# Kernel optimization log

Hardware: AMD Instinct MI355X
Metric: run time of the kernel (lower is better)

The kernel has to match this reference:

```python
import jax, jax.numpy as jnp
import numpy as np

EMBED_DIM = 768
MAX_LEN = 1024
ALPHA = 0.99
BATCH = 16


def setup_inputs() -> dict:
    key = jax.random.key(0)
    k1, k2, k3 = jax.random.split(key, 3)
    x = jax.random.normal(k1, (BATCH, MAX_LEN, EMBED_DIM), dtype=jnp.float32)
    # torch nn.Linear(embed_dim, 3*embed_dim): store weight as [in, out] for x @ W
    scale = 1.0 / np.sqrt(EMBED_DIM)
    W_qkv = jax.random.uniform(k2, (EMBED_DIM, 3 * EMBED_DIM), dtype=jnp.float32,
                               minval=-scale, maxval=scale)
    b_qkv = jax.random.uniform(k3, (3 * EMBED_DIM,), dtype=jnp.float32,
                               minval=-scale, maxval=scale)
    return {"x": x, "W_qkv": W_qkv, "b_qkv": b_qkv}


def _retention_mask(sl, alpha, dtype):
    # M[i, j] = alpha**(i - j) if i >= j else 0 (causal tril * decay)
    i = jnp.arange(sl)[:, None]
    j = jnp.arange(sl)[None, :]
    causal = i >= j
    # compute decay only where causal to avoid huge alpha**(negative) values
    exponent = jnp.where(causal, (i - j).astype(dtype), 0.0)
    decay = jnp.asarray(alpha, dtype) ** exponent
    return jnp.where(causal, decay, jnp.zeros((), dtype))


def reference(x, W_qkv, b_qkv):
    bs, sl, d = x.shape
    qkv = x @ W_qkv + b_qkv                      # [B, S, 3D]
    q, k, v = jnp.split(qkv, 3, axis=-1)         # each [B, S, D]
    M = _retention_mask(sl, ALPHA, x.dtype)      # [S, S]
    scores = jnp.einsum('bsd,btd->bst', q, k) / jnp.sqrt(jnp.asarray(d, x.dtype))
    out = jnp.einsum('bst,btd->bsd', scores * M[None, :, :], v)
    return out
```

## Files before the change

kernel.cpp:

```cpp
#include <hip/hip_runtime.h>
#include <hip/hip_bf16.h>


#define SEQ   1024
#define DIM   768
#define ND3   2304

typedef __attribute__((ext_vector_type(8))) short bf16x8;
typedef __attribute__((ext_vector_type(4))) float f32x4;

#define L2A     (-0.014499569695115089f)
#define RSQRTD  (0.03608439182435161f)

__device__ __forceinline__ unsigned short f2bf(float x) {
  union { float f; unsigned u; } v; v.f = x;
  unsigned r = v.u + 0x7FFFu + ((v.u >> 16) & 1u);
  return (unsigned short)(r >> 16);
}

__device__ __forceinline__ void gload16(const void* g, void* l) {
  __builtin_amdgcn_global_load_lds(
      (const __attribute__((address_space(1))) void*)g,
      (__attribute__((address_space(3))) void*)l, 16, 0, 0);
}

__device__ __forceinline__ void gemm_core(
    const unsigned short* gA, const unsigned short* gA2,
    const unsigned short* gB, const unsigned short* gB2,
    char* lsA, char* lsB, int nt, int wid, int lane, f32x4 acc[2][4]) {
  int lr = lane & 15, lg = lane >> 4;
  int wm = wid >> 1, wn = wid & 1;
  int rdA = (wm * 32 + lr) * 128 + ((lg ^ (lr & 7)) << 4);
  int rdB = (wn * 64 + lr) * 128 + ((lg ^ (lr & 7)) << 4);
  int wo = wid * 2048;

#define STAGE(t, par) do {                                                    \
    int lo_ = ((par) << 14) + wo;                                             \
    gload16(gA  + (size_t)(t) * 64, lsA + lo_);                               \
    gload16(gA2 + (size_t)(t) * 64, lsA + lo_ + 1024);                        \
    gload16(gB  + (size_t)(t) * 64, lsB + lo_);                               \
    gload16(gB2 + (size_t)(t) * 64, lsB + lo_ + 1024);                        \
  } while (0)

  STAGE(0, 0);
  STAGE(1, 1);
  asm volatile("s_waitcnt vmcnt(4)" ::: "memory");
  __builtin_amdgcn_s_barrier();
  asm volatile("" ::: "memory");

  for (int t = 0; t < nt; ++t) {
    int pbase = (t & 1) << 14;
    bf16x8 aF[2][2], bF[2][4];
#pragma unroll
    for (int kh = 0; kh < 2; ++kh) {
#pragma unroll
      for (int f = 0; f < 2; ++f)
        aF[kh][f] = *(const bf16x8*)(lsA + pbase + ((rdA + f * 2048) ^ (kh << 6)));
#pragma unroll
      for (int n = 0; n < 4; ++n)
        bF[kh][n] = *(const bf16x8*)(lsB + pbase + ((rdB + n * 2048) ^ (kh << 6)));
    }
    __builtin_amdgcn_s_setprio(1);
#pragma unroll
    for (int kh = 0; kh < 2; ++kh)
#pragma unroll
      for (int f = 0; f < 2; ++f)
#pragma unroll
        for (int n = 0; n < 4; ++n)
          acc[f][n] = __builtin_amdgcn_mfma_f32_16x16x32_bf16(aF[kh][f], bF[kh][n], acc[f][n], 0, 0, 0);
    __builtin_amdgcn_s_setprio(0);

    if (t == nt - 1) break;
    __builtin_amdgcn_s_barrier();
    asm volatile("" ::: "memory");
    if (t + 2 < nt) {
      STAGE(t + 2, t & 1);
      asm volatile("s_waitcnt vmcnt(4)" ::: "memory");
    } else {
      asm volatile("s_waitcnt vmcnt(0)" ::: "memory");
    }
    __builtin_amdgcn_s_barrier();
    asm volatile("" ::: "memory");
  }
#undef STAGE
}

__global__ void prep(const float* __restrict__ x, unsigned short* __restrict__ xb,
                     const float* __restrict__ W, unsigned short* __restrict__ Wt) {
  __shared__ float tile[64][65];
  int bid = blockIdx.x;
  if (bid < 6144) {
    size_t i = ((size_t)bid * 256 + threadIdx.x) * 8;
    float4 f0 = *(const float4*)(x + i);
    float4 f1 = *(const float4*)(x + i + 4);
    bf16x8 v;
    v[0] = (short)f2bf(f0.x); v[1] = (short)f2bf(f0.y);
    v[2] = (short)f2bf(f0.z); v[3] = (short)f2bf(f0.w);
    v[4] = (short)f2bf(f1.x); v[5] = (short)f2bf(f1.y);
    v[6] = (short)f2bf(f1.z); v[7] = (short)f2bf(f1.w);
    *(bf16x8*)(xb + i) = v;
  } else {
    int tb = bid - 6144;
    int n0 = (tb % 36) * 64;
    int k0 = (tb / 36) * 64;
    int tx = threadIdx.x & 63, ty = threadIdx.x >> 6;
#pragma unroll
    for (int p = 0; p < 16; ++p) {
      int k = ty + p * 4;
      tile[k][tx] = W[(size_t)(k0 + k) * ND3 + n0 + tx];
    }
    __syncthreads();
#pragma unroll
    for (int p = 0; p < 16; ++p) {
      int n = ty + p * 4;
      Wt[(size_t)(n0 + n) * DIM + k0 + tx] = f2bf(tile[tx][n]);
    }
  }
}

__global__ void __launch_bounds__(512, 4) qkv_g(
    const unsigned short* __restrict__ xb, const unsigned short* __restrict__ Wt,
    const float* __restrict__ bias,
    unsigned short* __restrict__ Qs, unsigned short* __restrict__ Ks,
    unsigned short* __restrict__ Vt) {
  __shared__ __align__(1024) char lsA[32768];
  __shared__ __align__(1024) char lsB[32768];
  int bid = (blockIdx.x & 7) * 288 + (blockIdx.x >> 3);
  int mt = bid / 18, ntb = bid % 18;
  int m0 = mt * 128, n0 = ntb * 128;

  int tid = threadIdx.x, lane = tid & 63, wid = tid >> 6;
  int l8 = lane >> 3, cs = ((lane & 7) ^ l8) << 3;
  int srow = wid * 16 + l8;

  const unsigned short* gA = xb + (size_t)(m0 + srow) * DIM + cs;
  const unsigned short* gB = Wt + (size_t)(n0 + srow) * DIM + cs;

  f32x4 acc[2][4] = {};
  gemm_core(gA, gA + 8 * DIM, gB, gB + 8 * DIM, lsA, lsB, 12, wid, lane, acc);

  int wm = wid >> 1, wn = wid & 1;
  int lr = lane & 15, lg = lane >> 4;
  float bia[4];
#pragma unroll
  for (int n = 0; n < 4; ++n) bia[n] = bias[n0 + wn * 64 + n * 16 + lr];

  if (ntb < 6) {
#pragma unroll
    for (int f = 0; f < 2; ++f)
#pragma unroll
      for (int r = 0; r < 4; ++r) {
        int mg = m0 + wm * 32 + f * 16 + lg * 4 + r;
        int b = mg >> 10, s = mg & 1023;
        float sc = exp2f((float)s * L2A) * RSQRTD;
        unsigned short* dst = Qs + ((size_t)b * SEQ + s) * DIM + n0 + wn * 64 + lr;
#pragma unroll
        for (int n = 0; n < 4; ++n)
          dst[n * 16] = f2bf((acc[f][n][r] + bia[n]) * sc);
      }
  } else if (ntb < 12) {
#pragma unroll
    for (int f = 0; f < 2; ++f)
#pragma unroll
      for (int r = 0; r < 4; ++r) {
        int mg = m0 + wm * 32 + f * 16 + lg * 4 + r;
        int b = mg >> 10, s = mg & 1023;
        float sc = exp2f(-(float)s * L2A);
        unsigned short* dst = Ks + ((size_t)b * SEQ + s) * DIM + (n0 - DIM) + wn * 64 + lr;
#pragma unroll
        for (int n = 0; n < 4; ++n)
          dst[n * 16] = f2bf((acc[f][n][r] + bia[n]) * sc);
      }
  } else {
#pragma unroll
    for (int f = 0; f < 2; ++f) {
      int mg = m0 + wm * 32 + f * 16 + lg * 4;
      int b = mg >> 10, s0 = mg & 1023;
#pragma unroll
      for (int n = 0; n < 4; ++n) {
        int d = (n0 - 2 * DIM) + wn * 64 + n * 16 + lr;
        ushort4 v;
        v.x = f2bf(acc[f][n][0] + bia[n]);
        v.y = f2bf(acc[f][n][1] + bia[n]);
        v.z = f2bf(acc[f][n][2] + bia[n]);
        v.w = f2bf(acc[f][n][3] + bia[n]);
        *(ushort4*)(Vt + ((size_t)b * DIM + d) * SEQ + s0) = v;
      }
    }
  }
}

__global__ void __launch_bounds__(512, 4) score_g(
    const unsigned short* __restrict__ Qs, const unsigned short* __restrict__ Ks,
    unsigned short* __restrict__ Sm, int b_base) {
  __shared__ __align__(1024) char lsA[32768];
  __shared__ __align__(1024) char lsB[32768];
  int bid = (blockIdx.x & 7) * (gridDim.x >> 3) + (blockIdx.x >> 3);
  int t = bid % 36, bl = bid / 36;
  int b = b_base + bl;
  int it = 0;
  while (t >= it + 1) { t -= it + 1; it++; }
  int jt = t;
  int m0 = it * 128, n0 = jt * 128;
  const unsigned short* A  = Qs + (size_t)b * SEQ * DIM;
  const unsigned short* Bt = Ks + (size_t)b * SEQ * DIM;
  unsigned short* Smp = Sm + (size_t)bl * SEQ * SEQ;

  int tid = threadIdx.x, lane = tid & 63, wid = tid >> 6;
  int l8 = lane >> 3, cs = ((lane & 7) ^ l8) << 3;
  int srow = wid * 16 + l8;

  const unsigned short* gA = A  + (size_t)(m0 + srow) * DIM + cs;
  const unsigned short* gB = Bt + (size_t)(n0 + srow) * DIM + cs;

  f32x4 acc[2][4] = {};
  gemm_core(gA, gA + 8 * DIM, gB, gB + 8 * DIM, lsA, lsB, 12, wid, lane, acc);

  int wm = wid >> 1, wn = wid & 1;
  int lr = lane & 15, lg = lane >> 4;
#pragma unroll
  for (int f = 0; f < 2; ++f)
#pragma unroll
    for (int n = 0; n < 4; ++n) {
      int j = n0 + wn * 64 + n * 16 + lr;
#pragma unroll
      for (int r = 0; r < 4; ++r) {
        int i = m0 + wm * 32 + f * 16 + lg * 4 + r;
        float v = acc[f][n][r];
        if (j > i) v = 0.0f;
        Smp[(size_t)i * SEQ + j] = f2bf(v);
      }
    }
}

__global__ void __launch_bounds__(512, 4) pv_g(
    const unsigned short* __restrict__ Sm, const unsigned short* __restrict__ Vt,
    float* __restrict__ out, int b_base, int gsz) {
  __shared__ __align__(1024) char lsA[32768];
  __shared__ __align__(1024) char lsB[32768];
  int xcd = blockIdx.x & 7;
  int j = blockIdx.x >> 3;
  int nbx = gsz >> 3;
  int perit = nbx * 6;
  int it = 7 - j / perit;
  int rem = j % perit;
  int bl = xcd * nbx + rem / 6;
  int dt = rem % 6;
  int b = b_base + bl;
  int m0 = it * 128, n0 = dt * 128;
  const unsigned short* A  = Sm + (size_t)bl * SEQ * SEQ;
  const unsigned short* Bt = Vt + (size_t)b * DIM * SEQ;
  int nt = (it + 1) * 2;

  int tid = threadIdx.x, lane = tid & 63, wid = tid >> 6;
  int l8 = lane >> 3, cs = ((lane & 7) ^ l8) << 3;
  int srow = wid * 16 + l8;

  const unsigned short* gA = A  + (size_t)(m0 + srow) * SEQ + cs;
  const unsigned short* gB = Bt + (size_t)(n0 + srow) * SEQ + cs;

  f32x4 acc[2][4] = {};
  gemm_core(gA, gA + 8 * SEQ, gB, gB + 8 * SEQ, lsA, lsB, nt, wid, lane, acc);

  int wm = wid >> 1, wn = wid & 1;
  int lr = lane & 15, lg = lane >> 4;
#pragma unroll
  for (int f = 0; f < 2; ++f)
#pragma unroll
    for (int n = 0; n < 4; ++n) {
      int d = n0 + wn * 64 + n * 16 + lr;
#pragma unroll
      for (int r = 0; r < 4; ++r) {
        int i = m0 + wm * 32 + f * 16 + lg * 4 + r;
        out[((size_t)b * SEQ + i) * DIM + d] = acc[f][n][r];
      }
    }
}

extern "C" void kernel_launch(void* const* d_in, const int* in_sizes, int n_in,
                              void* d_out, int out_size, void* d_ws, size_t ws_size,
                              hipStream_t stream) {
  const float* x    = (const float*)d_in[0];
  const float* W    = (const float*)d_in[1];
  const float* bias = (const float*)d_in[2];
  float* out = (float*)d_out;

  char* ws = (char*)d_ws;
  unsigned short* Wt = (unsigned short*)(ws);
  unsigned short* Qs = (unsigned short*)(ws + 3538944);
  unsigned short* Ks = (unsigned short*)(ws + 3538944 + 25165824);
  unsigned short* Vt = (unsigned short*)(ws + 3538944 + 2 * 25165824);
  unsigned short* Sm = (unsigned short*)(ws + 3538944 + 3 * 25165824);
  unsigned short* xb = (unsigned short*)d_out;

  size_t smBase = 3538944 + 3 * (size_t)25165824;
  int gsz = (ws_size >= smBase + (size_t)16 * SEQ * SEQ * 2) ? 16 : 8;
  int ngrp = 16 / gsz;

  prep<<<6576, 256, 0, stream>>>(x, xb, W, Wt);
  qkv_g<<<2304, 512, 0, stream>>>(xb, Wt, bias, Qs, Ks, Vt);
  for (int g = 0; g < ngrp; ++g) {
    score_g<<<gsz * 36, 512, 0, stream>>>(Qs, Ks, Sm, g * gsz);
    pv_g<<<gsz * 48, 512, 0, stream>>>(Sm, Vt, out, g * gsz, gsz);
  }
}
```

Baseline: 138.9 us.

## Fuse fp32-to-bf16 conversion of x into the QKV GEMM A-tile loading

Removes the separate pass that converted x to bf16 into a scratch buffer. The QKV GEMM now loads fp32 x directly into registers, converts it with packed bf16 conversion instructions, and writes swizzled tiles to LDS, with a hand-written double-buffered pipeline. This avoids a full write and re-read of the bf16 copy of x. The cost is doubled global read bytes for A, since each of the 18 column blocks re-reads fp32 x, plus register-staged loads and conversion work inside the GEMM loop.

```diff
diff --git a/kernel.cpp b/kernel.cpp
--- a/kernel.cpp
+++ b/kernel.cpp
@@ -85,41 +85,26 @@
 #undef STAGE
 }
 
-__global__ void prep(const float* __restrict__ x, unsigned short* __restrict__ xb,
-                     const float* __restrict__ W, unsigned short* __restrict__ Wt) {
+__global__ void transpose_w(const float* __restrict__ W, unsigned short* __restrict__ Wt) {
   __shared__ float tile[64][65];
-  int bid = blockIdx.x;
-  if (bid < 6144) {
-    size_t i = ((size_t)bid * 256 + threadIdx.x) * 8;
-    float4 f0 = *(const float4*)(x + i);
-    float4 f1 = *(const float4*)(x + i + 4);
-    bf16x8 v;
-    v[0] = (short)f2bf(f0.x); v[1] = (short)f2bf(f0.y);
-    v[2] = (short)f2bf(f0.z); v[3] = (short)f2bf(f0.w);
-    v[4] = (short)f2bf(f1.x); v[5] = (short)f2bf(f1.y);
-    v[6] = (short)f2bf(f1.z); v[7] = (short)f2bf(f1.w);
-    *(bf16x8*)(xb + i) = v;
-  } else {
-    int tb = bid - 6144;
-    int n0 = (tb % 36) * 64;
-    int k0 = (tb / 36) * 64;
-    int tx = threadIdx.x & 63, ty = threadIdx.x >> 6;
-#pragma unroll
-    for (int p = 0; p < 16; ++p) {
-      int k = ty + p * 4;
-      tile[k][tx] = W[(size_t)(k0 + k) * ND3 + n0 + tx];
-    }
-    __syncthreads();
-#pragma unroll
-    for (int p = 0; p < 16; ++p) {
-      int n = ty + p * 4;
-      Wt[(size_t)(n0 + n) * DIM + k0 + tx] = f2bf(tile[tx][n]);
-    }
+  int n0 = (blockIdx.x % 36) * 64;
+  int k0 = (blockIdx.x / 36) * 64;
+  int tx = threadIdx.x & 63, ty = threadIdx.x >> 6;
+#pragma unroll
+  for (int p = 0; p < 16; ++p) {
+    int k = ty + p * 4;
+    tile[k][tx] = W[(size_t)(k0 + k) * ND3 + n0 + tx];
+  }
+  __syncthreads();
+#pragma unroll
+  for (int p = 0; p < 16; ++p) {
+    int n = ty + p * 4;
+    Wt[(size_t)(n0 + n) * DIM + k0 + tx] = f2bf(tile[tx][n]);
   }
 }
 
 __global__ void __launch_bounds__(512, 4) qkv_g(
-    const unsigned short* __restrict__ xb, const unsigned short* __restrict__ Wt,
+    const float* __restrict__ x, const unsigned short* __restrict__ Wt,
     const float* __restrict__ bias,
     unsigned short* __restrict__ Qs, unsigned short* __restrict__ Ks,
     unsigned short* __restrict__ Vt) {
@@ -130,17 +115,101 @@
   int m0 = mt * 128, n0 = ntb * 128;
 
   int tid = threadIdx.x, lane = tid & 63, wid = tid >> 6;
-  int l8 = lane >> 3, cs = ((lane & 7) ^ l8) << 3;
-  int srow = wid * 16 + l8;
-
-  const unsigned short* gA = xb + (size_t)(m0 + srow) * DIM + cs;
-  const unsigned short* gB = Wt + (size_t)(n0 + srow) * DIM + cs;
+  int lr = lane & 15, lg = lane >> 4;
+  int wm = wid >> 1, wn = wid & 1;
+
+  int l8 = lane >> 3, csB = ((lane & 7) ^ l8) << 3;
+  const unsigned short* gB  = Wt + (size_t)(n0 + wid * 16 + l8) * DIM + csB;
+  const unsigned short* gB2 = gB + (size_t)8 * DIM;
+  const float* gAf = x + (size_t)(m0 + wid * 16 + (lane >> 2)) * DIM + (lane & 3) * 16;
+  int arow = wid * 16 + (lane >> 2);
+  int awr0 = arow * 128 + ((((lane & 3) * 2)     ^ (arow & 7)) << 4);
+  int awr1 = arow * 128 + ((((lane & 3) * 2 + 1) ^ (arow & 7)) << 4);
+  int rdA = (wm * 32 + lr) * 128 + ((lg ^ (lr & 7)) << 4);
+  int rdB = (wn * 64 + lr) * 128 + ((lg ^ (lr & 7)) << 4);
 
   f32x4 acc[2][4] = {};
-  gemm_core(gA, gA + 8 * DIM, gB, gB + 8 * DIM, lsA, lsB, 12, wid, lane, acc);
-
-  int wm = wid >> 1, wn = wid & 1;
-  int lr = lane & 15, lg = lane >> 4;
+
+#define ISSUE(t, f0, f1, f2, f3) do {                                         \
+    const float* s_ = gAf + (t) * 64;                                         \
+    f0 = *(const float4*)(s_);                                                \
+    f1 = *(const float4*)(s_ + 4);                                            \
+    f2 = *(const float4*)(s_ + 8);                                            \
+    f3 = *(const float4*)(s_ + 12);                                           \
+    gload16(gB  + (size_t)(t) * 64, lsB + (((t) & 1) << 14) + wid * 2048);    \
+    gload16(gB2 + (size_t)(t) * 64, lsB + (((t) & 1) << 14) + wid * 2048 + 1024);\
+  } while (0)
+#define CVT8(dst, fa, fb) do {                                                \
+    unsigned q0_, q1_, q2_, q3_;                                              \
+    asm("v_cvt_pk_bf16_f32 %0, %1, %2" : "=v"(q0_) : "v"(fa.x), "v"(fa.y));   \
+    asm("v_cvt_pk_bf16_f32 %0, %1, %2" : "=v"(q1_) : "v"(fa.z), "v"(fa.w));   \
+    asm("v_cvt_pk_bf16_f32 %0, %1, %2" : "=v"(q2_) : "v"(fb.x), "v"(fb.y));   \
+    asm("v_cvt_pk_bf16_f32 %0, %1, %2" : "=v"(q3_) : "v"(fb.z), "v"(fb.w));   \
+    *(uint4*)(dst) = make_uint4(q0_, q1_, q2_, q3_);                          \
+  } while (0)
+#define WRITE_A(par, f0, f1, f2, f3) do {                                     \
+    CVT8(lsA + ((par) << 14) + awr0, f0, f1);                                 \
+    CVT8(lsA + ((par) << 14) + awr1, f2, f3);                                 \
+  } while (0)
+#define COMPUTE(par) do {                                                     \
+    int pbase_ = (par) << 14;                                                 \
+    bf16x8 aF[2][2], bF[2][4];                                                \
+    _Pragma("unroll")                                                         \
+    for (int kh = 0; kh < 2; ++kh) {                                          \
+      _Pragma("unroll")                                                       \
+      for (int f = 0; f < 2; ++f)                                             \
+        aF[kh][f] = *(const bf16x8*)(lsA + pbase_ + ((rdA + f * 2048) ^ (kh << 6)));\
+      _Pragma("unroll")                                                       \
+      for (int n = 0; n < 4; ++n)                                             \
+        bF[kh][n] = *(const bf16x8*)(lsB + pbase_ + ((rdB + n * 2048) ^ (kh << 6)));\
+    }                                                                         \
+    __builtin_amdgcn_s_setprio(1);                                            \
+    _Pragma("unroll")                                                         \
+    for (int kh = 0; kh < 2; ++kh)                                            \
+      _Pragma("unroll")                                                       \
+      for (int f = 0; f < 2; ++f)                                             \
+        _Pragma("unroll")                                                     \
+        for (int n = 0; n < 4; ++n)                                           \
+          acc[f][n] = __builtin_amdgcn_mfma_f32_16x16x32_bf16(aF[kh][f], bF[kh][n], acc[f][n], 0, 0, 0);\
+    __builtin_amdgcn_s_setprio(0);                                            \
+  } while (0)
+#define BARRIER do { __builtin_amdgcn_s_barrier(); asm volatile("" ::: "memory"); } while (0)
+
+  float4 x0, x1, x2, x3, y0, y1, y2, y3;
+  ISSUE(0, x0, x1, x2, x3);
+  ISSUE(1, y0, y1, y2, y3);
+  asm volatile("s_waitcnt vmcnt(6)" ::: "memory");
+  WRITE_A(0, x0, x1, x2, x3);
+  asm volatile("s_waitcnt lgkmcnt(0)" ::: "memory");
+  BARRIER;
+
+  for (int tt = 0; tt < 6; ++tt) {
+    COMPUTE(0);
+    BARRIER;
+    if (tt < 5) {
+      ISSUE(2 * tt + 2, x0, x1, x2, x3);
+      asm volatile("s_waitcnt vmcnt(6)" ::: "memory");
+    } else {
+      asm volatile("s_waitcnt vmcnt(0)" ::: "memory");
+    }
+    WRITE_A(1, y0, y1, y2, y3);
+    asm volatile("s_waitcnt lgkmcnt(0)" ::: "memory");
+    BARRIER;
+    COMPUTE(1);
+    if (tt == 5) break;
+    BARRIER;
+    ISSUE(2 * tt + 3, y0, y1, y2, y3);
+    asm volatile("s_waitcnt vmcnt(6)" ::: "memory");
+    WRITE_A(0, x0, x1, x2, x3);
+    asm volatile("s_waitcnt lgkmcnt(0)" ::: "memory");
+    BARRIER;
+  }
+#undef ISSUE
+#undef CVT8
+#undef WRITE_A
+#undef COMPUTE
+#undef BARRIER
+
   float bia[4];
 #pragma unroll
   for (int n = 0; n < 4; ++n) bia[n] = bias[n0 + wn * 64 + n * 16 + lr];
@@ -291,14 +360,13 @@
   unsigned short* Ks = (unsigned short*)(ws + 3538944 + 25165824);
   unsigned short* Vt = (unsigned short*)(ws + 3538944 + 2 * 25165824);
   unsigned short* Sm = (unsigned short*)(ws + 3538944 + 3 * 25165824);
-  unsigned short* xb = (unsigned short*)d_out;
 
   size_t smBase = 3538944 + 3 * (size_t)25165824;
   int gsz = (ws_size >= smBase + (size_t)16 * SEQ * SEQ * 2) ? 16 : 8;
   int ngrp = 16 / gsz;
 
-  prep<<<6576, 256, 0, stream>>>(x, xb, W, Wt);
-  qkv_g<<<2304, 512, 0, stream>>>(xb, Wt, bias, Qs, Ks, Vt);
+  transpose_w<<<432, 256, 0, stream>>>(W, Wt);
+  qkv_g<<<2304, 512, 0, stream>>>(x, Wt, bias, Qs, Ks, Vt);
   for (int g = 0; g < ngrp; ++g) {
     score_g<<<gsz * 36, 512, 0, stream>>>(Qs, Ks, Sm, g * gsz);
     pv_g<<<gsz * 48, 512, 0, stream>>>(Sm, Vt, out, g * gsz, gsz);
```

Measured after the change: 155.8 us. 12.1% more time.
